# Kernel optimization log

Hardware: AMD Instinct MI355X
Metric: run time of the kernel (lower is better)

Reference implementation:

```python
import jax, jax.numpy as jnp
import numpy as np


def setup_inputs() -> dict:
    key = jax.random.key(0)
    ks = jax.random.split(key, 7)
    B, C, W, H = 4, 256, 64, 64
    C8 = C // 8
    return {
        "x": jax.random.normal(ks[0], (B, C, W, H), dtype=jnp.float32),
        "Wq": jax.random.normal(ks[1], (C8, C), dtype=jnp.float32) * 0.05,
        "bq": jax.random.normal(ks[2], (C8,), dtype=jnp.float32) * 0.05,
        "Wk": jax.random.normal(ks[3], (C8, C), dtype=jnp.float32) * 0.05,
        "bk": jax.random.normal(ks[4], (C8,), dtype=jnp.float32) * 0.05,
        "Wv": jax.random.normal(ks[5], (C, C), dtype=jnp.float32) * 0.05,
        "bv": jax.random.normal(ks[6], (C,), dtype=jnp.float32) * 0.05,
    }


def reference(x, Wq, bq, Wk, bk, Wv, bv):
    B, C, W, H = x.shape
    N = W * H
    xf = x.reshape(B, C, N)  # flatten spatial dims
    # 1x1 convs == per-position linear projections
    q = jnp.einsum('oc,bcn->bno', Wq, xf) + bq            # (B, N, C/8)
    k = jnp.einsum('oc,bcn->bon', Wk, xf) + bk[None, :, None]  # (B, C/8, N)
    # attention scores (B, N, N); original applies softmax over dim=1
    attn = jax.nn.softmax(jnp.einsum('bno,bom->bnm', q, k), axis=1)
    v = jnp.einsum('oc,bcn->bno', Wv, xf) + bv            # (B, N, C)
    out = jnp.einsum('bnm,bmc->bnc', attn, v)             # (B, N, C)
    # faithful to original: raw view of (B, N, C) as (B, C, W, H)
    return out.reshape(B, C, W, H)
```

## Files before the change

kernel.cpp:

```cpp
#include <hip/hip_runtime.h>
#include <math.h>

#define NB 4
#define CC 256
#define CO 32
#define NN 4096
#define MU 320
#define LOG2E 1.44269504088896f

typedef __attribute__((ext_vector_type(4))) float f4;
typedef __attribute__((ext_vector_type(8))) short s8;
typedef __attribute__((ext_vector_type(8))) unsigned short us8;
typedef __attribute__((ext_vector_type(2))) unsigned int u2;
typedef __attribute__((ext_vector_type(4))) unsigned int u4i;

__device__ __forceinline__ unsigned short f2bf(float f) {
    unsigned int u = __float_as_uint(f);
    u = (u + 0x7FFFu + ((u >> 16) & 1u)) >> 16;
    return (unsigned short)u;
}
__device__ __forceinline__ unsigned int cvtpk(float lo, float hi) {
    unsigned int r;
    asm("v_cvt_pk_bf16_f32 %0, %1, %2" : "=v"(r) : "v"(lo), "v"(hi));
    return r;
}
__device__ __forceinline__ int swz128(int row, int colByte) {
    return row * 128 + (colByte ^ ((row & 7) << 4));
}
#define LDS_BARRIER() asm volatile("s_waitcnt lgkmcnt(0)\n\ts_barrier" ::: "memory")

union s8u4 { s8 s; u4i u; };

__global__ __launch_bounds__(256) void prepw_kernel(
    const float* __restrict__ Wq, const float* __restrict__ bq,
    const float* __restrict__ Wk, const float* __restrict__ bk,
    const float* __restrict__ Wv, const float* __restrict__ bv,
    unsigned short* __restrict__ Wb, float* __restrict__ fb)
{
    const int t = threadIdx.x;
    #pragma unroll
    for (int i = 0; i < 4; ++i) {
        const int e = blockIdx.x * 1024 + i * 256 + t;
        const int u = e >> 8, c = e & 255;
        float val = (u < 32) ? Wq[u * 256 + c]
                  : (u < 64) ? Wk[(u - 32) * 256 + c]
                             : Wv[(u - 64) * 256 + c];
        Wb[e] = f2bf(val);
    }
    if (blockIdx.x == 0) {
        for (int u = t; u < MU; u += 256)
            fb[u] = (u < 32) ? bq[u] : (u < 64) ? bk[u - 32] : bv[u - 64];
    }
}

__global__ __launch_bounds__(256) void projf_kernel(
    const float* __restrict__ x, const unsigned short* __restrict__ Wb,
    const float* __restrict__ fb,
    unsigned short* __restrict__ qb, unsigned short* __restrict__ kb,
    unsigned short* __restrict__ vtb)
{
    __shared__ float xl[32][260];

    const int t   = threadIdx.x;
    const int b   = blockIdx.x >> 7;
    const int nbl = blockIdx.x & 127;
    const int n0  = nbl * 32;

    {
        const int nl = t & 7;
        const int c8 = t >> 3;
        #pragma unroll
        for (int pass = 0; pass < 8; ++pass) {
            const int c = c8 + pass * 32;
            f4 xv = *reinterpret_cast<const f4*>(x + ((size_t)(b * CC + c)) * NN + n0 + nl * 4);
            #pragma unroll
            for (int j = 0; j < 4; ++j) xl[nl * 4 + j][c] = xv[j];
        }
    }
    __syncthreads();

    const int w    = t >> 6;
    const int l    = t & 63;
    const int l15  = l & 15;
    const int g4   = l >> 4;
    const int nw   = w & 1;
    const int uw   = w >> 1;
    const int nloc = nw * 16 + l15;
    const int n    = n0 + nloc;

    s8 bfr[8];
    #pragma unroll
    for (int kk = 0; kk < 8; ++kk) {
        f4 a  = *reinterpret_cast<const f4*>(&xl[nloc][kk * 32 + g4 * 8]);
        f4 c2 = *reinterpret_cast<const f4*>(&xl[nloc][kk * 32 + g4 * 8 + 4]);
        s8u4 tmp;
        tmp.u = (u4i){ cvtpk(a[0], a[1]), cvtpk(a[2], a[3]),
                       cvtpk(c2[0], c2[1]), cvtpk(c2[2], c2[3]) };
        bfr[kk] = tmp.s;
    }

    const f4 z = {0.f, 0.f, 0.f, 0.f};
    unsigned short* qrow = qb + ((size_t)(b * NN + n)) * CO;
    unsigned short* krow = kb + ((size_t)(b * NN + n)) * CO;

    #pragma unroll
    for (int i = 0; i < 10; ++i) {
        const int u0 = (uw * 10 + i) * 16;
        f4 acc = z;
        #pragma unroll
        for (int kk = 0; kk < 8; ++kk) {
            s8 af = *reinterpret_cast<const s8*>(Wb + (size_t)(u0 + l15) * CC + kk * 32 + g4 * 8);
            acc = __builtin_amdgcn_mfma_f32_16x16x32_bf16(af, bfr[kk], acc, 0, 0, 0);
        }
        f4 bias4 = *reinterpret_cast<const f4*>(fb + u0 + g4 * 4);
        if (u0 < 32) {
            u2 pw = { cvtpk((acc[0] + bias4[0]) * LOG2E, (acc[1] + bias4[1]) * LOG2E),
                      cvtpk((acc[2] + bias4[2]) * LOG2E, (acc[3] + bias4[3]) * LOG2E) };
            *reinterpret_cast<u2*>(qrow + u0 + g4 * 4) = pw;
        } else if (u0 < 64) {
            u2 pw = { cvtpk(acc[0] + bias4[0], acc[1] + bias4[1]),
                      cvtpk(acc[2] + bias4[2], acc[3] + bias4[3]) };
            *reinterpret_cast<u2*>(krow + (u0 - 32) + g4 * 4) = pw;
        } else {
            const int cbase = u0 - 64 + g4 * 4;
            #pragma unroll
            for (int r = 0; r < 4; ++r)
                vtb[((size_t)(b * CC + cbase + r)) * NN + n] = f2bf(acc[r] + bias4[r]);
        }
    }
}

__global__ __launch_bounds__(256) void colstats_kernel(
    const unsigned short* __restrict__ qb, const unsigned short* __restrict__ kb,
    const unsigned short* __restrict__ vtb, unsigned short* __restrict__ vfr)
{
    __shared__ float red[4][16];
    __shared__ float civl[16];

    const int t   = threadIdx.x;
    const int b   = blockIdx.x >> 8;
    const int mb  = blockIdx.x & 255;
    const int l   = t & 63;
    const int w   = t >> 6;
    const int l15 = l & 15;
    const int g4  = l >> 4;
    const int m   = mb * 16 + l15;

    const unsigned short* qbB = qb + (size_t)b * NN * CO;
    s8 kfrag = *reinterpret_cast<const s8*>(kb + ((size_t)b * NN + m) * CO + g4 * 8);

    const f4 z = {0.f, 0.f, 0.f, 0.f};
    float ssum = 0.f;

    const int nbeg = w * 1024, nend = nbeg + 1024;
    for (int n0 = nbeg; n0 < nend; n0 += 32) {
        s8 a0 = *reinterpret_cast<const s8*>(qbB + (size_t)(n0 + l15) * CO + g4 * 8);
        s8 a1 = *reinterpret_cast<const s8*>(qbB + (size_t)(n0 + 16 + l15) * CO + g4 * 8);
        f4 d0 = __builtin_amdgcn_mfma_f32_16x16x32_bf16(a0, kfrag, z, 0, 0, 0);
        f4 d1 = __builtin_amdgcn_mfma_f32_16x16x32_bf16(a1, kfrag, z, 0, 0, 0);
        #pragma unroll
        for (int r = 0; r < 4; ++r) ssum += exp2f(d0[r]) + exp2f(d1[r]);
    }

    ssum += __shfl_xor(ssum, 16);
    ssum += __shfl_xor(ssum, 32);
    if (l < 16) red[w][l15] = ssum;
    __syncthreads();
    if (w == 0 && l < 16)
        civl[l15] = 1.0f / (red[0][l15] + red[1][l15] + red[2][l15] + red[3][l15]);
    __syncthreads();

    const int mt   = mb >> 2;
    const int ksl  = (mb >> 1) & 1;
    const int g4b  = (mb & 1) * 2;
    const int cg   = t >> 4;
    const int l15v = t & 15;
    const unsigned short* vp = vtb + ((size_t)(b * CC + t)) * NN + mb * 16;
    unsigned short* dst = vfr + (size_t)b * 1048576
                        + (((mt * 16 + cg) * 2 + ksl) << 9)
                        + (g4b * 16 + l15v) * 8;
    #pragma unroll
    for (int i = 0; i < 2; ++i) {
        us8 vv = *reinterpret_cast<const us8*>(vp + i * 8);
        u4i o;
        #pragma unroll
        for (int e2 = 0; e2 < 4; ++e2) {
            float f0 = __uint_as_float((unsigned int)vv[2 * e2]     << 16) * civl[i * 8 + 2 * e2];
            float f1 = __uint_as_float((unsigned int)vv[2 * e2 + 1] << 16) * civl[i * 8 + 2 * e2 + 1];
            o[e2] = cvtpk(f0, f1);
        }
        *reinterpret_cast<u4i*>(dst + i * 128) = o;
    }
}

__global__ __launch_bounds__(512) void attn_kernel(
    const unsigned short* __restrict__ qb, const unsigned short* __restrict__ kb,
    const unsigned short* __restrict__ vfr, float* __restrict__ out)
{
    __shared__ __align__(16) char plds[2][64 * 128];

    const int t    = threadIdx.x;
    const int bid  = blockIdx.x;
    const int cblk = bid & 1;
    const int nblk = (bid >> 1) & 63;
    const int b    = bid >> 7;
    const int n0   = nblk * 64;
    const int c0   = cblk * 128;
    const int l    = t & 63;
    const int w    = t >> 6;
    const int l15  = l & 15;
    const int g4   = l >> 4;
    const int g    = w >> 1;
    const int p    = w & 1;
    const int wrn  = w >> 2;
    const int wcq  = w & 3;

    const unsigned short* qbB = qb  + (size_t)b * NN * CO;
    const unsigned short* kbB = kb  + (size_t)b * NN * CO;

    s8 qfrag = *reinterpret_cast<const s8*>(qbB + (size_t)(n0 + g * 16 + l15) * CO + g4 * 8);

    const int pw0  = swz128(g * 16 + l15, (2 * p) * 32 + g4 * 8);
    const int pw1  = swz128(g * 16 + l15, (2 * p + 1) * 32 + g4 * 8);
    const int prk0a0 = swz128(wrn * 32 +      l15,      g4 * 16);
    const int prk0a1 = swz128(wrn * 32 + 16 + l15,      g4 * 16);
    const int prk1a0 = swz128(wrn * 32 +      l15, 64 + g4 * 16);
    const int prk1a1 = swz128(wrn * 32 + 16 + l15, 64 + g4 * 16);

    const unsigned short* kp  = kbB + (size_t)((2 * p) * 16 + l15) * CO + g4 * 8;
    const unsigned short* vpf = vfr + (size_t)b * 1048576
                              + (size_t)((c0 >> 4) + wcq * 2) * 1024 + l * 8;

    s8 kreg[2];
    s8 vA0, vA1, vA2, vA3, vB0, vB1, vB2, vB3;
    const f4 z = {0.f, 0.f, 0.f, 0.f};

#define LOADK() do { \
        kreg[0] = *reinterpret_cast<const s8*>(kp); \
        kreg[1] = *reinterpret_cast<const s8*>(kp + 16 * CO); \
        kp += 64 * CO; \
    } while (0)

#define LOADVB(V0, V1, V2, V3) do { \
        V0 = *reinterpret_cast<const s8*>(vpf); \
        V1 = *reinterpret_cast<const s8*>(vpf + 512); \
        V2 = *reinterpret_cast<const s8*>(vpf + 1024); \
        V3 = *reinterpret_cast<const s8*>(vpf + 1536); \
        vpf += 16384; \
    } while (0)

#define STAGE(BUF) do { \
        f4 d0 = __builtin_amdgcn_mfma_f32_16x16x32_bf16(kreg[0], qfrag, z, 0, 0, 0); \
        f4 d1 = __builtin_amdgcn_mfma_f32_16x16x32_bf16(kreg[1], qfrag, z, 0, 0, 0); \
        u2 pq0 = { cvtpk(exp2f(d0[0]), exp2f(d0[1])), cvtpk(exp2f(d0[2]), exp2f(d0[3])) }; \
        u2 pq1 = { cvtpk(exp2f(d1[0]), exp2f(d1[1])), cvtpk(exp2f(d1[2]), exp2f(d1[3])) }; \
        *reinterpret_cast<u2*>(plds[BUF] + pw0) = pq0; \
        *reinterpret_cast<u2*>(plds[BUF] + pw1) = pq1; \
    } while (0)

#define PVSTEP(BUF, V0, V1, V2, V3) do { \
        s8 pa00 = *reinterpret_cast<const s8*>(plds[BUF] + prk0a0); \
        s8 pa01 = *reinterpret_cast<const s8*>(plds[BUF] + prk0a1); \
        s8 pa10 = *reinterpret_cast<const s8*>(plds[BUF] + prk1a0); \
        s8 pa11 = *reinterpret_cast<const s8*>(plds[BUF] + prk1a1); \
        __builtin_amdgcn_s_setprio(1); \
        acc[0][0] = __builtin_amdgcn_mfma_f32_16x16x32_bf16(pa00, V0, acc[0][0], 0, 0, 0); \
        acc[0][1] = __builtin_amdgcn_mfma_f32_16x16x32_bf16(pa00, V2, acc[0][1], 0, 0, 0); \
        acc[1][0] = __builtin_amdgcn_mfma_f32_16x16x32_bf16(pa01, V0, acc[1][0], 0, 0, 0); \
        acc[1][1] = __builtin_amdgcn_mfma_f32_16x16x32_bf16(pa01, V2, acc[1][1], 0, 0, 0); \
        acc[0][0] = __builtin_amdgcn_mfma_f32_16x16x32_bf16(pa10, V1, acc[0][0], 0, 0, 0); \
        acc[0][1] = __builtin_amdgcn_mfma_f32_16x16x32_bf16(pa10, V3, acc[0][1], 0, 0, 0); \
        acc[1][0] = __builtin_amdgcn_mfma_f32_16x16x32_bf16(pa11, V1, acc[1][0], 0, 0, 0); \
        acc[1][1] = __builtin_amdgcn_mfma_f32_16x16x32_bf16(pa11, V3, acc[1][1], 0, 0, 0); \
        __builtin_amdgcn_s_setprio(0); \
    } while (0)

    f4 acc[2][2];
    acc[0][0] = z; acc[0][1] = z; acc[1][0] = z; acc[1][1] = z;

    LOADK();
    LOADVB(vA0, vA1, vA2, vA3);
    STAGE(0);
    LOADK();
    LOADVB(vB0, vB1, vB2, vB3);
    LDS_BARRIER();

    for (int i = 0; i < 64; i += 2) {
        if (i < 63) {
            STAGE(1);
            if (i < 62) LOADK();
        }
        PVSTEP(0, vA0, vA1, vA2, vA3);
        if (i < 62) LOADVB(vA0, vA1, vA2, vA3);
        LDS_BARRIER();

        if (i + 1 < 63) {
            STAGE(0);
            if (i + 1 < 62) LOADK();
        }
        PVSTEP(1, vB0, vB1, vB2, vB3);
        if (i + 1 < 62) LOADVB(vB0, vB1, vB2, vB3);
        LDS_BARRIER();
    }

#undef LOADK
#undef LOADVB
#undef STAGE
#undef PVSTEP

    #pragma unroll
    for (int a = 0; a < 2; ++a) {
        const int row = n0 + wrn * 32 + a * 16 + g4 * 4;
        #pragma unroll
        for (int c = 0; c < 2; ++c) {
            const int col = c0 + wcq * 32 + c * 16 + l15;
            #pragma unroll
            for (int r = 0; r < 4; ++r)
                out[((size_t)(b * NN + row + r)) * CC + col] = acc[a][c][r];
        }
    }
}

extern "C" void kernel_launch(void* const* d_in, const int* in_sizes, int n_in,
                              void* d_out, int out_size, void* d_ws, size_t ws_size,
                              hipStream_t stream)
{
    const float* x  = (const float*)d_in[0];
    const float* Wq = (const float*)d_in[1];
    const float* bq = (const float*)d_in[2];
    const float* Wk = (const float*)d_in[3];
    const float* bk = (const float*)d_in[4];
    const float* Wv = (const float*)d_in[5];
    const float* bv = (const float*)d_in[6];
    float* out = (float*)d_out;

    unsigned short* qb  = (unsigned short*)d_ws;
    unsigned short* kb  = qb  + (size_t)NB * NN * CO;
    unsigned short* vtb = kb  + (size_t)NB * NN * CO;
    unsigned short* vfr = vtb + (size_t)NB * CC * NN;
    unsigned short* Wb  = vfr + (size_t)NB * CC * NN;
    float*          fb  = (float*)(Wb + (size_t)MU * CC);

    prepw_kernel<<<dim3(80), dim3(256), 0, stream>>>(Wq, bq, Wk, bk, Wv, bv, Wb, fb);
    projf_kernel<<<dim3(512), dim3(256), 0, stream>>>(x, Wb, fb, qb, kb, vtb);
    colstats_kernel<<<dim3(1024), dim3(256), 0, stream>>>(qb, kb, vtb, vfr);
    attn_kernel<<<dim3(512), dim3(512), 0, stream>>>(qb, kb, vfr, out);
}
```

Measured before the change: 122.2 us.

## Stage V tiles through LDS cooperatively and deepen K/V prefetch

V fragments were previously loaded per wave straight from global memory, and waves sharing a column slice loaded duplicate data. Now all threads cooperatively load each V tile once, store it into a double-buffered LDS region alongside P, and each wave reads its MFMA operands from LDS. K and V global loads are also split into A/B register sets prefetched two stages ahead. This cuts redundant global traffic and lengthens load latency hiding, at the cost of extra LDS writes and reads, 32KB more shared memory, and more registers.

```diff
diff --git a/kernel.cpp b/kernel.cpp
--- a/kernel.cpp
+++ b/kernel.cpp
@@ -198,6 +198,7 @@
     const unsigned short* __restrict__ vfr, float* __restrict__ out)
 {
     __shared__ __align__(16) char plds[2][64 * 128];
+    __shared__ __align__(16) char vlds[2][16384];
 
     const int t    = threadIdx.x;
     const int bid  = blockIdx.x;
@@ -226,85 +227,90 @@
     const int prk0a1 = swz128(wrn * 32 + 16 + l15,      g4 * 16);
     const int prk1a0 = swz128(wrn * 32 +      l15, 64 + g4 * 16);
     const int prk1a1 = swz128(wrn * 32 + 16 + l15, 64 + g4 * 16);
-
-    const unsigned short* kp  = kbB + (size_t)((2 * p) * 16 + l15) * CO + g4 * 8;
-    const unsigned short* vpf = vfr + (size_t)b * 1048576
-                              + (size_t)((c0 >> 4) + wcq * 2) * 1024 + l * 8;
-
-    s8 kreg[2];
-    s8 vA0, vA1, vA2, vA3, vB0, vB1, vB2, vB3;
+    const int vw0 = t * 16;
+    const int vw1 = 8192 + t * 16;
+    const int vrb = wcq * 4096 + l * 16;
+
+    const unsigned short* kpA = kbB + (size_t)((2 * p) * 16 + l15) * CO + g4 * 8;
+    const unsigned short* kpB = kpA + (size_t)64 * CO;
+    const unsigned short* vpA = vfr + (size_t)b * 1048576 + (size_t)(c0 >> 4) * 1024 + t * 8;
+    const unsigned short* vpB = vpA + 16384;
+
+    s8 kA0, kA1, kB0, kB1;
+    s8 vA0, vA1, vB0, vB1;
     const f4 z = {0.f, 0.f, 0.f, 0.f};
 
-#define LOADK() do { \
-        kreg[0] = *reinterpret_cast<const s8*>(kp); \
-        kreg[1] = *reinterpret_cast<const s8*>(kp + 16 * CO); \
-        kp += 64 * CO; \
+#define LOADA() do { \
+        kA0 = *reinterpret_cast<const s8*>(kpA); \
+        kA1 = *reinterpret_cast<const s8*>(kpA + 16 * CO); \
+        vA0 = *reinterpret_cast<const s8*>(vpA); \
+        vA1 = *reinterpret_cast<const s8*>(vpA + 4096); \
+        kpA += 128 * CO; vpA += 32768; \
     } while (0)
 
-#define LOADVB(V0, V1, V2, V3) do { \
-        V0 = *reinterpret_cast<const s8*>(vpf); \
-        V1 = *reinterpret_cast<const s8*>(vpf + 512); \
-        V2 = *reinterpret_cast<const s8*>(vpf + 1024); \
-        V3 = *reinterpret_cast<const s8*>(vpf + 1536); \
-        vpf += 16384; \
+#define LOADB() do { \
+        kB0 = *reinterpret_cast<const s8*>(kpB); \
+        kB1 = *reinterpret_cast<const s8*>(kpB + 16 * CO); \
+        vB0 = *reinterpret_cast<const s8*>(vpB); \
+        vB1 = *reinterpret_cast<const s8*>(vpB + 4096); \
+        kpB += 128 * CO; vpB += 32768; \
     } while (0)
 
-#define STAGE(BUF) do { \
-        f4 d0 = __builtin_amdgcn_mfma_f32_16x16x32_bf16(kreg[0], qfrag, z, 0, 0, 0); \
-        f4 d1 = __builtin_amdgcn_mfma_f32_16x16x32_bf16(kreg[1], qfrag, z, 0, 0, 0); \
+#define STAGE(BUF, K0, K1, V0, V1) do { \
+        f4 d0 = __builtin_amdgcn_mfma_f32_16x16x32_bf16(K0, qfrag, z, 0, 0, 0); \
+        f4 d1 = __builtin_amdgcn_mfma_f32_16x16x32_bf16(K1, qfrag, z, 0, 0, 0); \
         u2 pq0 = { cvtpk(exp2f(d0[0]), exp2f(d0[1])), cvtpk(exp2f(d0[2]), exp2f(d0[3])) }; \
         u2 pq1 = { cvtpk(exp2f(d1[0]), exp2f(d1[1])), cvtpk(exp2f(d1[2]), exp2f(d1[3])) }; \
         *reinterpret_cast<u2*>(plds[BUF] + pw0) = pq0; \
         *reinterpret_cast<u2*>(plds[BUF] + pw1) = pq1; \
+        *reinterpret_cast<s8*>(vlds[BUF] + vw0) = V0; \
+        *reinterpret_cast<s8*>(vlds[BUF] + vw1) = V1; \
     } while (0)
 
-#define PVSTEP(BUF, V0, V1, V2, V3) do { \
+#define PVSTEP(BUF) do { \
         s8 pa00 = *reinterpret_cast<const s8*>(plds[BUF] + prk0a0); \
         s8 pa01 = *reinterpret_cast<const s8*>(plds[BUF] + prk0a1); \
         s8 pa10 = *reinterpret_cast<const s8*>(plds[BUF] + prk1a0); \
         s8 pa11 = *reinterpret_cast<const s8*>(plds[BUF] + prk1a1); \
+        s8 vb00 = *reinterpret_cast<const s8*>(vlds[BUF] + vrb); \
+        s8 vb10 = *reinterpret_cast<const s8*>(vlds[BUF] + vrb + 1024); \
+        s8 vb01 = *reinterpret_cast<const s8*>(vlds[BUF] + vrb + 2048); \
+        s8 vb11 = *reinterpret_cast<const s8*>(vlds[BUF] + vrb + 3072); \
         __builtin_amdgcn_s_setprio(1); \
-        acc[0][0] = __builtin_amdgcn_mfma_f32_16x16x32_bf16(pa00, V0, acc[0][0], 0, 0, 0); \
-        acc[0][1] = __builtin_amdgcn_mfma_f32_16x16x32_bf16(pa00, V2, acc[0][1], 0, 0, 0); \
-        acc[1][0] = __builtin_amdgcn_mfma_f32_16x16x32_bf16(pa01, V0, acc[1][0], 0, 0, 0); \
-        acc[1][1] = __builtin_amdgcn_mfma_f32_16x16x32_bf16(pa01, V2, acc[1][1], 0, 0, 0); \
-        acc[0][0] = __builtin_amdgcn_mfma_f32_16x16x32_bf16(pa10, V1, acc[0][0], 0, 0, 0); \
-        acc[0][1] = __builtin_amdgcn_mfma_f32_16x16x32_bf16(pa10, V3, acc[0][1], 0, 0, 0); \
-        acc[1][0] = __builtin_amdgcn_mfma_f32_16x16x32_bf16(pa11, V1, acc[1][0], 0, 0, 0); \
-        acc[1][1] = __builtin_amdgcn_mfma_f32_16x16x32_bf16(pa11, V3, acc[1][1], 0, 0, 0); \
+        acc[0][0] = __builtin_amdgcn_mfma_f32_16x16x32_bf16(pa00, vb00, acc[0][0], 0, 0, 0); \
+        acc[0][1] = __builtin_amdgcn_mfma_f32_16x16x32_bf16(pa00, vb01, acc[0][1], 0, 0, 0); \
+        acc[1][0] = __builtin_amdgcn_mfma_f32_16x16x32_bf16(pa01, vb00, acc[1][0], 0, 0, 0); \
+        acc[1][1] = __builtin_amdgcn_mfma_f32_16x16x32_bf16(pa01, vb01, acc[1][1], 0, 0, 0); \
+        acc[0][0] = __builtin_amdgcn_mfma_f32_16x16x32_bf16(pa10, vb10, acc[0][0], 0, 0, 0); \
+        acc[0][1] = __builtin_amdgcn_mfma_f32_16x16x32_bf16(pa10, vb11, acc[0][1], 0, 0, 0); \
+        acc[1][0] = __builtin_amdgcn_mfma_f32_16x16x32_bf16(pa11, vb10, acc[1][0], 0, 0, 0); \
+        acc[1][1] = __builtin_amdgcn_mfma_f32_16x16x32_bf16(pa11, vb11, acc[1][1], 0, 0, 0); \
         __builtin_amdgcn_s_setprio(0); \
     } while (0)
 
     f4 acc[2][2];
     acc[0][0] = z; acc[0][1] = z; acc[1][0] = z; acc[1][1] = z;
 
-    LOADK();
-    LOADVB(vA0, vA1, vA2, vA3);
-    STAGE(0);
-    LOADK();
-    LOADVB(vB0, vB1, vB2, vB3);
+    LOADA();
+    LOADB();
+    STAGE(0, kA0, kA1, vA0, vA1);
+    LOADA();
     LDS_BARRIER();
 
     for (int i = 0; i < 64; i += 2) {
-        if (i < 63) {
-            STAGE(1);
-            if (i < 62) LOADK();
-        }
-        PVSTEP(0, vA0, vA1, vA2, vA3);
-        if (i < 62) LOADVB(vA0, vA1, vA2, vA3);
+        STAGE(1, kB0, kB1, vB0, vB1);
+        if (i + 3 < 64) LOADB();
+        PVSTEP(0);
         LDS_BARRIER();
 
-        if (i + 1 < 63) {
-            STAGE(0);
-            if (i + 1 < 62) LOADK();
-        }
-        PVSTEP(1, vB0, vB1, vB2, vB3);
-        if (i + 1 < 62) LOADVB(vB0, vB1, vB2, vB3);
+        if (i + 2 < 64) STAGE(0, kA0, kA1, vA0, vA1);
+        if (i + 4 < 64) LOADA();
+        PVSTEP(1);
         LDS_BARRIER();
     }
 
-#undef LOADK
-#undef LOADVB
+#undef LOADA
+#undef LOADB
 #undef STAGE
 #undef PVSTEP
 
```

Result: no change. 122.6 us (+0.3%).

## Retile attention kernel to 32 query rows by full channels with XCD-aware block order

Applied to the files above, without the earlier changes.

Each block now covers 32 query rows and all 256 output channels instead of 64 rows by 128 channels. The QK^T and exp work is no longer duplicated across two channel blocks, each wave does one score MFMA per step, and the LDS tile is halved. Block IDs are remapped so consecutive launches of the same batch land on the same XCD, and launch bounds request higher occupancy. In exchange, every block streams the full V for its batch, so total V traffic doubles, and the register cap from the occupancy hint may cause spills.

```diff
diff --git a/kernel.cpp b/kernel.cpp
--- a/kernel.cpp
+++ b/kernel.cpp
@@ -193,131 +193,110 @@
     }
 }
 
-__global__ __launch_bounds__(512) void attn_kernel(
+__global__ __launch_bounds__(512, 4) void attn_kernel(
     const unsigned short* __restrict__ qb, const unsigned short* __restrict__ kb,
     const unsigned short* __restrict__ vfr, float* __restrict__ out)
 {
-    __shared__ __align__(16) char plds[2][64 * 128];
-
-    const int t    = threadIdx.x;
-    const int bid  = blockIdx.x;
-    const int cblk = bid & 1;
-    const int nblk = (bid >> 1) & 63;
+    __shared__ __align__(16) char plds[2][32 * 128];
+
+    const int t   = threadIdx.x;
+    const int w   = t >> 6;
+    const int l   = t & 63;
+    const int l15 = l & 15;
+    const int g4  = l >> 4;
+    const int bid  = (blockIdx.x & 7) * 64 + (blockIdx.x >> 3);
     const int b    = bid >> 7;
-    const int n0   = nblk * 64;
-    const int c0   = cblk * 128;
-    const int l    = t & 63;
-    const int w    = t >> 6;
-    const int l15  = l & 15;
-    const int g4   = l >> 4;
-    const int g    = w >> 1;
-    const int p    = w & 1;
-    const int wrn  = w >> 2;
-    const int wcq  = w & 3;
-
-    const unsigned short* qbB = qb  + (size_t)b * NN * CO;
-    const unsigned short* kbB = kb  + (size_t)b * NN * CO;
-
-    s8 qfrag = *reinterpret_cast<const s8*>(qbB + (size_t)(n0 + g * 16 + l15) * CO + g4 * 8);
-
-    const int pw0  = swz128(g * 16 + l15, (2 * p) * 32 + g4 * 8);
-    const int pw1  = swz128(g * 16 + l15, (2 * p + 1) * 32 + g4 * 8);
-    const int prk0a0 = swz128(wrn * 32 +      l15,      g4 * 16);
-    const int prk0a1 = swz128(wrn * 32 + 16 + l15,      g4 * 16);
-    const int prk1a0 = swz128(wrn * 32 +      l15, 64 + g4 * 16);
-    const int prk1a1 = swz128(wrn * 32 + 16 + l15, 64 + g4 * 16);
-
-    const unsigned short* kp  = kbB + (size_t)((2 * p) * 16 + l15) * CO + g4 * 8;
-    const unsigned short* vpf = vfr + (size_t)b * 1048576
-                              + (size_t)((c0 >> 4) + wcq * 2) * 1024 + l * 8;
-
-    s8 kreg[2];
-    s8 vA0, vA1, vA2, vA3, vB0, vB1, vB2, vB3;
+    const int nblk = bid & 127;
+    const int n0   = nblk * 32;
+    const int ng   = w >> 2;
+    const int mq   = w & 3;
+
+    const unsigned short* qbB = qb + (size_t)b * NN * CO;
+    const unsigned short* kbB = kb + (size_t)b * NN * CO;
+
+    s8 qfrag = *reinterpret_cast<const s8*>(qbB + (size_t)(n0 + ng * 16 + l15) * CO + g4 * 8);
+
+    const int pwo  = swz128(ng * 16 + l15, mq * 32 + g4 * 8);
+    const int pr00 = swz128(l15,      g4 * 16);
+    const int pr01 = swz128(l15,      64 + g4 * 16);
+    const int pr10 = swz128(16 + l15, g4 * 16);
+    const int pr11 = swz128(16 + l15, 64 + g4 * 16);
+
+    const unsigned short* kp = kbB + (size_t)(mq * 16 + l15) * CO + g4 * 8;
+    const unsigned short* vp = vfr + (size_t)b * 1048576 + w * 2048 + l * 8;
+
+    s8 kreg;
+    s8 v0, v1, v2, v3;
     const f4 z = {0.f, 0.f, 0.f, 0.f};
-
-#define LOADK() do { \
-        kreg[0] = *reinterpret_cast<const s8*>(kp); \
-        kreg[1] = *reinterpret_cast<const s8*>(kp + 16 * CO); \
-        kp += 64 * CO; \
+    f4 acc00 = z, acc01 = z, acc10 = z, acc11 = z;
+
+#define LOADK() do { kreg = *reinterpret_cast<const s8*>(kp); kp += 2048; } while (0)
+#define LOADV() do { \
+        v0 = *reinterpret_cast<const s8*>(vp); \
+        v1 = *reinterpret_cast<const s8*>(vp + 512); \
+        v2 = *reinterpret_cast<const s8*>(vp + 1024); \
+        v3 = *reinterpret_cast<const s8*>(vp + 1536); \
+        vp += 16384; \
     } while (0)
 
-#define LOADVB(V0, V1, V2, V3) do { \
-        V0 = *reinterpret_cast<const s8*>(vpf); \
-        V1 = *reinterpret_cast<const s8*>(vpf + 512); \
-        V2 = *reinterpret_cast<const s8*>(vpf + 1024); \
-        V3 = *reinterpret_cast<const s8*>(vpf + 1536); \
-        vpf += 16384; \
+#define STAGE(BUF, KR) do { \
+        f4 d = __builtin_amdgcn_mfma_f32_16x16x32_bf16(KR, qfrag, z, 0, 0, 0); \
+        u2 pw = { cvtpk(exp2f(d[0]), exp2f(d[1])), cvtpk(exp2f(d[2]), exp2f(d[3])) }; \
+        *reinterpret_cast<u2*>(plds[BUF] + pwo) = pw; \
     } while (0)
 
-#define STAGE(BUF) do { \
-        f4 d0 = __builtin_amdgcn_mfma_f32_16x16x32_bf16(kreg[0], qfrag, z, 0, 0, 0); \
-        f4 d1 = __builtin_amdgcn_mfma_f32_16x16x32_bf16(kreg[1], qfrag, z, 0, 0, 0); \
-        u2 pq0 = { cvtpk(exp2f(d0[0]), exp2f(d0[1])), cvtpk(exp2f(d0[2]), exp2f(d0[3])) }; \
-        u2 pq1 = { cvtpk(exp2f(d1[0]), exp2f(d1[1])), cvtpk(exp2f(d1[2]), exp2f(d1[3])) }; \
-        *reinterpret_cast<u2*>(plds[BUF] + pw0) = pq0; \
-        *reinterpret_cast<u2*>(plds[BUF] + pw1) = pq1; \
-    } while (0)
-
-#define PVSTEP(BUF, V0, V1, V2, V3) do { \
-        s8 pa00 = *reinterpret_cast<const s8*>(plds[BUF] + prk0a0); \
-        s8 pa01 = *reinterpret_cast<const s8*>(plds[BUF] + prk0a1); \
-        s8 pa10 = *reinterpret_cast<const s8*>(plds[BUF] + prk1a0); \
-        s8 pa11 = *reinterpret_cast<const s8*>(plds[BUF] + prk1a1); \
+#define PVSTEP(BUF) do { \
+        s8 pa00 = *reinterpret_cast<const s8*>(plds[BUF] + pr00); \
+        s8 pa01 = *reinterpret_cast<const s8*>(plds[BUF] + pr01); \
+        s8 pa10 = *reinterpret_cast<const s8*>(plds[BUF] + pr10); \
+        s8 pa11 = *reinterpret_cast<const s8*>(plds[BUF] + pr11); \
         __builtin_amdgcn_s_setprio(1); \
-        acc[0][0] = __builtin_amdgcn_mfma_f32_16x16x32_bf16(pa00, V0, acc[0][0], 0, 0, 0); \
-        acc[0][1] = __builtin_amdgcn_mfma_f32_16x16x32_bf16(pa00, V2, acc[0][1], 0, 0, 0); \
-        acc[1][0] = __builtin_amdgcn_mfma_f32_16x16x32_bf16(pa01, V0, acc[1][0], 0, 0, 0); \
-        acc[1][1] = __builtin_amdgcn_mfma_f32_16x16x32_bf16(pa01, V2, acc[1][1], 0, 0, 0); \
-        acc[0][0] = __builtin_amdgcn_mfma_f32_16x16x32_bf16(pa10, V1, acc[0][0], 0, 0, 0); \
-        acc[0][1] = __builtin_amdgcn_mfma_f32_16x16x32_bf16(pa10, V3, acc[0][1], 0, 0, 0); \
-        acc[1][0] = __builtin_amdgcn_mfma_f32_16x16x32_bf16(pa11, V1, acc[1][0], 0, 0, 0); \
-        acc[1][1] = __builtin_amdgcn_mfma_f32_16x16x32_bf16(pa11, V3, acc[1][1], 0, 0, 0); \
+        acc00 = __builtin_amdgcn_mfma_f32_16x16x32_bf16(pa00, v0, acc00, 0, 0, 0); \
+        acc01 = __builtin_amdgcn_mfma_f32_16x16x32_bf16(pa00, v2, acc01, 0, 0, 0); \
+        acc10 = __builtin_amdgcn_mfma_f32_16x16x32_bf16(pa10, v0, acc10, 0, 0, 0); \
+        acc11 = __builtin_amdgcn_mfma_f32_16x16x32_bf16(pa10, v2, acc11, 0, 0, 0); \
+        acc00 = __builtin_amdgcn_mfma_f32_16x16x32_bf16(pa01, v1, acc00, 0, 0, 0); \
+        acc01 = __builtin_amdgcn_mfma_f32_16x16x32_bf16(pa01, v3, acc01, 0, 0, 0); \
+        acc10 = __builtin_amdgcn_mfma_f32_16x16x32_bf16(pa11, v1, acc10, 0, 0, 0); \
+        acc11 = __builtin_amdgcn_mfma_f32_16x16x32_bf16(pa11, v3, acc11, 0, 0, 0); \
         __builtin_amdgcn_s_setprio(0); \
     } while (0)
 
-    f4 acc[2][2];
-    acc[0][0] = z; acc[0][1] = z; acc[1][0] = z; acc[1][1] = z;
-
+    s8 k0 = *reinterpret_cast<const s8*>(kp); kp += 2048;
     LOADK();
-    LOADVB(vA0, vA1, vA2, vA3);
-    STAGE(0);
-    LOADK();
-    LOADVB(vB0, vB1, vB2, vB3);
+    LOADV();
+    STAGE(0, k0);
     LDS_BARRIER();
 
     for (int i = 0; i < 64; i += 2) {
-        if (i < 63) {
-            STAGE(1);
-            if (i < 62) LOADK();
-        }
-        PVSTEP(0, vA0, vA1, vA2, vA3);
-        if (i < 62) LOADVB(vA0, vA1, vA2, vA3);
+        STAGE(1, kreg);
+        if (i < 62) LOADK();
+        PVSTEP(0);
+        if (i < 63) LOADV();
         LDS_BARRIER();
 
-        if (i + 1 < 63) {
-            STAGE(0);
-            if (i + 1 < 62) LOADK();
-        }
-        PVSTEP(1, vB0, vB1, vB2, vB3);
-        if (i + 1 < 62) LOADVB(vB0, vB1, vB2, vB3);
+        if (i + 1 < 63) STAGE(0, kreg);
+        if (i + 1 < 62) LOADK();
+        PVSTEP(1);
+        if (i + 1 < 63) LOADV();
         LDS_BARRIER();
     }
 
 #undef LOADK
-#undef LOADVB
+#undef LOADV
 #undef STAGE
 #undef PVSTEP
 
-    #pragma unroll
-    for (int a = 0; a < 2; ++a) {
-        const int row = n0 + wrn * 32 + a * 16 + g4 * 4;
-        #pragma unroll
-        for (int c = 0; c < 2; ++c) {
-            const int col = c0 + wcq * 32 + c * 16 + l15;
-            #pragma unroll
-            for (int r = 0; r < 4; ++r)
-                out[((size_t)(b * NN + row + r)) * CC + col] = acc[a][c][r];
-        }
+    float* ob = out + (size_t)b * NN * CC;
+    const int cw = w * 32 + l15;
+    #pragma unroll
+    for (int r = 0; r < 4; ++r) {
+        const size_t row0 = (size_t)(n0 + g4 * 4 + r) * CC;
+        const size_t row1 = (size_t)(n0 + 16 + g4 * 4 + r) * CC;
+        ob[row0 + cw]      = acc00[r];
+        ob[row0 + cw + 16] = acc01[r];
+        ob[row1 + cw]      = acc10[r];
+        ob[row1 + cw + 16] = acc11[r];
     }
 }
 
```

New measurement: 112.0 us. 8.4% less time.
